# Kernel tuning notes

Hardware: AMD Instinct MI355X
Metric: run time of the kernel (lower is better)

The kernel has to match this reference:

```python
import jax, jax.numpy as jnp
import numpy as np

B, S, H = 512, 200, 256

def setup_inputs() -> dict:
    key = jax.random.key(0)
    ks = jax.random.split(key, 7)
    scale = 1.0 / np.sqrt(H)
    return {
        "all_memory": jax.random.normal(ks[0], (B, S, H), dtype=jnp.float32),
        "last_memory": jax.random.normal(ks[1], (B, H), dtype=jnp.float32),
        "U": jax.random.normal(ks[2], (H, H), dtype=jnp.float32) * scale,   # U_meta weight
        "W": jax.random.normal(ks[3], (H, H), dtype=jnp.float32) * scale,   # W_meta weight
        "V": jax.random.normal(ks[4], (H, 1), dtype=jnp.float32) * scale,   # V_meta weight (stored as [H,1])
        "MetaW": jax.random.normal(ks[5], (4, H), dtype=jnp.float32) * scale,  # Meta weight
        "Metab": jax.random.normal(ks[6], (4,), dtype=jnp.float32) * scale,    # Meta bias ('multiple' mode)
    }

def reference(all_memory, last_memory, U, W, V, MetaW, Metab):
    # U_meta(all_memory): [B,S,H]; W_meta(last_memory): [B,H] broadcast over S
    a = jnp.einsum('bsh,kh->bsk', all_memory, U)
    l = jnp.einsum('bh,kh->bk', last_memory, W)
    # additive attention score: V_meta(tanh(a + l)) -> [B,S]
    scores = jnp.einsum('bsh,h->bs', jnp.tanh(a + l[:, None, :]), V[:, 0])
    alpha = jax.nn.softmax(scores, axis=1)  # softmax over seq dim
    pooled = jnp.einsum('bs,bsh->bh', alpha, all_memory)  # weighted sum of values
    return pooled @ MetaW.T + Metab  # [B, 4]
```

## Files before the change

### kernel.cpp

```cpp
#include <hip/hip_runtime.h>
#include <hip/hip_bf16.h>
#include <math.h>

#define NB 512
#define NS 200
#define NH 256
#define TILE_S 32
#define LDSPAD 8
#define LDW (NH + LDSPAD)

#define OFF_L    0
#define OFF_UB   (NB * NH)
#define WS_FLOATS_PRE  (OFF_UB + (NH * NH) / 2)

typedef _Float16 f16x8 __attribute__((ext_vector_type(8)));
typedef float    f32x4 __attribute__((ext_vector_type(4)));

template<int CTRL>
__device__ __forceinline__ float dpp_xadd(float v) {
  return v + __int_as_float(
      __builtin_amdgcn_update_dpp(0, __float_as_int(v), CTRL, 0xf, 0xf, true));
}
__device__ __forceinline__ float row16_sum(float v) {
  v = dpp_xadd<0xB1>(v);
  v = dpp_xadd<0x4E>(v);
  v = dpp_xadd<0x124>(v);
  v = dpp_xadd<0x128>(v);
  return v;
}

__global__ __launch_bounds__(256)
void precompute(const float* __restrict__ lastm, const float* __restrict__ W,
                const float* __restrict__ U,
                float* __restrict__ l_ws, _Float16* __restrict__ Uswz)
{
  const int t = threadIdx.x;
  if (blockIdx.x < NB) {
    const int b = blockIdx.x;
    __shared__ float lm_sm[NH];
    lm_sm[t] = lastm[(size_t)b * NH + t];
    __syncthreads();
    const float4* wrow = (const float4*)(W + (size_t)t * NH);
    const float4* lrow = (const float4*)lm_sm;
    float a0 = 0.f, a1 = 0.f, a2 = 0.f, a3 = 0.f;
#pragma unroll 8
    for (int i = 0; i < NH / 4; ++i) {
      float4 w4 = wrow[i];
      float4 m4 = lrow[i];
      a0 = fmaf(w4.x, m4.x, a0);
      a1 = fmaf(w4.y, m4.y, a1);
      a2 = fmaf(w4.z, m4.z, a2);
      a3 = fmaf(w4.w, m4.w, a3);
    }
    l_ws[(size_t)b * NH + t] = (a0 + a1) + (a2 + a3);
  } else {
    const int id    = (blockIdx.x - NB) * 256 + t;
    const int n_blk = id >> 9;
    const int kk    = (id >> 6) & 7;
    const int lane  = id & 63;
    const int row   = n_blk * 16 + (lane & 15);
    const int col   = kk * 32 + (lane >> 4) * 8;
    const float4* s = (const float4*)(U + (size_t)row * NH + col);
    const float4 a = s[0], c = s[1];
    f16x8 pk;
    pk[0] = (_Float16)a.x; pk[1] = (_Float16)a.y;
    pk[2] = (_Float16)a.z; pk[3] = (_Float16)a.w;
    pk[4] = (_Float16)c.x; pk[5] = (_Float16)c.y;
    pk[6] = (_Float16)c.z; pk[7] = (_Float16)c.w;
    *(f16x8*)(Uswz + (size_t)id * 8) = pk;
  }
}

#define CVT_HL(idx, val) { const float x_ = (val); const _Float16 h_ = (_Float16)x_; \
                           ph[idx] = h_; pl[idx] = (_Float16)(x_ - (float)h_); }

template<bool PRE>
__global__ __launch_bounds__(512, 2)
void fused_attn(const float* __restrict__ mem,
                const float* __restrict__ lastm,
                const float* __restrict__ U,
                const float* __restrict__ W,
                const float* __restrict__ V,
                const float* __restrict__ l_ws,
                const _Float16* __restrict__ Uswz,
                const float* __restrict__ MetaW,
                const float* __restrict__ Metab,
                float* __restrict__ out)
{
  const int b = blockIdx.x;
  const int ntiles = 7;

  const int t     = threadIdx.x;
  const int wave  = t >> 6;
  const int lane  = t & 63;
  const int m16   = lane & 15;
  const int quad  = lane >> 4;
  const int g     = t >> 5;
  const int hblk  = (t & 31) * 8;

  __shared__ __align__(16) _Float16 hi_sm[2][TILE_S][LDW];
  __shared__ __align__(16) _Float16 lo_sm[2][TILE_S][LDW];
  __shared__ float swave_sm[8][TILE_S];
  __shared__ float e_sm[TILE_S];
  __shared__ float mz_sm[2];

  float l_reg[2], v_reg[2];
  if constexpr (!PRE) {
    __shared__ float l_sm[NH];
    __shared__ float lm_sm[NH];
    if (t < NH) lm_sm[t] = lastm[(size_t)b * NH + t];
    __syncthreads();
    if (t < NH) {
      const float4* wrow = (const float4*)(W + (size_t)t * NH);
      const float4* lrow = (const float4*)lm_sm;
      float a0 = 0.f, a1 = 0.f, a2 = 0.f, a3 = 0.f;
#pragma unroll 8
      for (int i = 0; i < NH / 4; ++i) {
        float4 w4 = wrow[i];
        float4 m4 = lrow[i];
        a0 = fmaf(w4.x, m4.x, a0);
        a1 = fmaf(w4.y, m4.y, a1);
        a2 = fmaf(w4.z, m4.z, a2);
        a3 = fmaf(w4.w, m4.w, a3);
      }
      l_sm[t] = (a0 + a1) + (a2 + a3);
    }
    __syncthreads();
#pragma unroll
    for (int nf = 0; nf < 2; ++nf)
      l_reg[nf] = l_sm[wave * 32 + nf * 16 + m16];
  } else {
#pragma unroll
    for (int nf = 0; nf < 2; ++nf)
      l_reg[nf] = l_ws[(size_t)b * NH + wave * 32 + nf * 16 + m16];
  }
#pragma unroll
  for (int nf = 0; nf < 2; ++nf)
    v_reg[nf] = V[wave * 32 + nf * 16 + m16];
  const float vsum  = v_reg[0] + v_reg[1];
  const float vm2_0 = -2.f * v_reg[0];
  const float vm2_1 = -2.f * v_reg[1];

  f16x8 u_frag[2][8];
  if constexpr (PRE) {
    const _Float16* uw = Uswz + ((size_t)(wave * 2 * 8 * 64) + lane) * 8;
#pragma unroll
    for (int nf = 0; nf < 2; ++nf)
#pragma unroll
      for (int kk = 0; kk < 8; ++kk)
        u_frag[nf][kk] = *(const f16x8*)(uw + (size_t)((nf * 8 + kk) << 9));
  } else {
#pragma unroll
    for (int nf = 0; nf < 2; ++nf) {
      const int n = wave * 32 + nf * 16 + m16;
      const float* urow = U + (size_t)n * NH;
#pragma unroll
      for (int kk = 0; kk < 8; ++kk) {
        const float4 lo = *(const float4*)(urow + kk * 32 + quad * 8);
        const float4 hi = *(const float4*)(urow + kk * 32 + quad * 8 + 4);
        f16x8 f;
        f[0] = (_Float16)lo.x; f[1] = (_Float16)lo.y;
        f[2] = (_Float16)lo.z; f[3] = (_Float16)lo.w;
        f[4] = (_Float16)hi.x; f[5] = (_Float16)hi.y;
        f[6] = (_Float16)hi.z; f[7] = (_Float16)hi.w;
        u_frag[nf][kk] = f;
      }
    }
  }

  {
    const float4* src4 = (const float4*)(mem + (size_t)b * NS * NH);
    const int f0 = t, f1 = 512 + t;
    const float4 a0 = src4[f0 * 2], a1 = src4[f0 * 2 + 1];
    const float4 b0 = src4[f1 * 2], b1 = src4[f1 * 2 + 1];
    {
      f16x8 ph, pl;
      CVT_HL(0, a0.x) CVT_HL(1, a0.y) CVT_HL(2, a0.z) CVT_HL(3, a0.w)
      CVT_HL(4, a1.x) CVT_HL(5, a1.y) CVT_HL(6, a1.z) CVT_HL(7, a1.w)
      *(f16x8*)&hi_sm[0][f0 >> 5][(f0 & 31) * 8] = ph;
      *(f16x8*)&lo_sm[0][f0 >> 5][(f0 & 31) * 8] = pl;
    }
    {
      f16x8 ph, pl;
      CVT_HL(0, b0.x) CVT_HL(1, b0.y) CVT_HL(2, b0.z) CVT_HL(3, b0.w)
      CVT_HL(4, b1.x) CVT_HL(5, b1.y) CVT_HL(6, b1.z) CVT_HL(7, b1.w)
      *(f16x8*)&hi_sm[0][f1 >> 5][(f1 & 31) * 8] = ph;
      *(f16x8*)&lo_sm[0][f1 >> 5][(f1 & 31) * 8] = pl;
    }
  }
  __syncthreads();

  float m_run = -INFINITY;
  float Z     = 0.f;
  float pooledv[8];
#pragma unroll
  for (int j = 0; j < 8; ++j) pooledv[j] = 0.f;

  for (int tile = 0; tile < ntiles; ++tile) {
    const int cur = tile & 1;
    const int nxt = cur ^ 1;
    const int s0  = tile * TILE_S;
    const int rows = min(TILE_S, NS - s0);
    const int rows_next = (tile + 1 < ntiles) ? min(TILE_S, NS - (s0 + TILE_S)) : 0;

    float4 p00, p01, p10, p11;
    const bool ld0 = (t >> 5) < rows_next;
    const bool ld1 = 16 + (t >> 5) < rows_next;
    {
      const float4* nsrc = (const float4*)(mem + ((size_t)b * NS + s0 + TILE_S) * NH);
      if (ld0) { p00 = nsrc[t * 2];         p01 = nsrc[t * 2 + 1]; }
      if (ld1) { p10 = nsrc[(512 + t) * 2]; p11 = nsrc[(512 + t) * 2 + 1]; }
    }

    f32x4 acc[2][2];
    const f32x4 fzero = {0.f, 0.f, 0.f, 0.f};
#pragma unroll
    for (int mt = 0; mt < 2; ++mt)
#pragma unroll
      for (int nf = 0; nf < 2; ++nf)
        acc[mt][nf] = fzero;

#pragma unroll
    for (int kk = 0; kk < 8; ++kk) {
      const int c = kk * 32 + quad * 8;
      f16x8 a0h = *(const f16x8*)&hi_sm[cur][m16][c];
      f16x8 a1h = *(const f16x8*)&hi_sm[cur][16 + m16][c];
      f16x8 a0l = *(const f16x8*)&lo_sm[cur][m16][c];
      f16x8 a1l = *(const f16x8*)&lo_sm[cur][16 + m16][c];
#pragma unroll
      for (int nf = 0; nf < 2; ++nf) {
        acc[0][nf] = __builtin_amdgcn_mfma_f32_16x16x32_f16(a0h, u_frag[nf][kk], acc[0][nf], 0, 0, 0);
        acc[1][nf] = __builtin_amdgcn_mfma_f32_16x16x32_f16(a1h, u_frag[nf][kk], acc[1][nf], 0, 0, 0);
        acc[0][nf] = __builtin_amdgcn_mfma_f32_16x16x32_f16(a0l, u_frag[nf][kk], acc[0][nf], 0, 0, 0);
        acc[1][nf] = __builtin_amdgcn_mfma_f32_16x16x32_f16(a1l, u_frag[nf][kk], acc[1][nf], 0, 0, 0);
      }
    }

#pragma unroll
    for (int mt = 0; mt < 2; ++mt) {
#pragma unroll
      for (int reg = 0; reg < 4; ++reg) {
        const float x0 = acc[mt][0][reg] + l_reg[0];
        const float x1 = acc[mt][1][reg] + l_reg[1];
        const float e0 = __expf(x0 + x0);
        const float e1 = __expf(x1 + x1);
        float s = vsum;
        s += __fdividef(vm2_0, e0 + 1.f);
        s += __fdividef(vm2_1, e1 + 1.f);
        s = row16_sum(s);
        if (m16 == 0)
          swave_sm[wave][mt * 16 + quad * 4 + reg] = s;
      }
    }
    __syncthreads();

    if (t < TILE_S) {
      float s = swave_sm[0][t];
#pragma unroll
      for (int w = 1; w < 8; ++w) s += swave_sm[w][t];
      const float sv = (t < rows) ? s : -INFINITY;
      float mt_ = sv;
#pragma unroll
      for (int off = 1; off < 32; off <<= 1)
        mt_ = fmaxf(mt_, __shfl_xor(mt_, off));
      const float m_new = fmaxf(m_run, mt_);
      float e = (t < rows) ? __expf(sv - m_new) : 0.f;
      e_sm[t] = e;
      float z = e;
#pragma unroll
      for (int off = 1; off < 32; off <<= 1)
        z += __shfl_xor(z, off);
      if (t == 0) { mz_sm[0] = m_new; mz_sm[1] = z; }
    }

    if (ld0) {
      f16x8 ph, pl;
      CVT_HL(0, p00.x) CVT_HL(1, p00.y) CVT_HL(2, p00.z) CVT_HL(3, p00.w)
      CVT_HL(4, p01.x) CVT_HL(5, p01.y) CVT_HL(6, p01.z) CVT_HL(7, p01.w)
      *(f16x8*)&hi_sm[nxt][t >> 5][(t & 31) * 8] = ph;
      *(f16x8*)&lo_sm[nxt][t >> 5][(t & 31) * 8] = pl;
    }
    if (ld1) {
      f16x8 ph, pl;
      CVT_HL(0, p10.x) CVT_HL(1, p10.y) CVT_HL(2, p10.z) CVT_HL(3, p10.w)
      CVT_HL(4, p11.x) CVT_HL(5, p11.y) CVT_HL(6, p11.z) CVT_HL(7, p11.w)
      *(f16x8*)&hi_sm[nxt][16 + (t >> 5)][(t & 31) * 8] = ph;
      *(f16x8*)&lo_sm[nxt][16 + (t >> 5)][(t & 31) * 8] = pl;
    }
    __syncthreads();

    const float m_new = mz_sm[0];
    const float z_new = mz_sm[1];
    const float fac   = __expf(m_run - m_new);
    m_run = m_new;
    Z = fmaf(Z, fac, z_new);

    const float e0 = e_sm[2 * g];
    const float e1 = e_sm[2 * g + 1];
    const f16x8 r0 = *(const f16x8*)&hi_sm[cur][2 * g][hblk];
    const f16x8 r1 = *(const f16x8*)&hi_sm[cur][2 * g + 1][hblk];
#pragma unroll
    for (int j = 0; j < 8; ++j)
      pooledv[j] = fmaf(e0, (float)r0[j], fmaf(e1, (float)r1[j], pooledv[j] * fac));
    __syncthreads();
  }

  float* scratch = (float*)&hi_sm[0][0][0];
  float* pooled_sm = (float*)&lo_sm[0][0][0];
  {
    f32x4 lo4 = {pooledv[0], pooledv[1], pooledv[2], pooledv[3]};
    f32x4 hi4 = {pooledv[4], pooledv[5], pooledv[6], pooledv[7]};
    *(f32x4*)&scratch[g * 264 + hblk]     = lo4;
    *(f32x4*)&scratch[g * 264 + hblk + 4] = hi4;
  }
  __syncthreads();
  const float Zi = 1.f / Z;
  if (t < NH) {
    float p = 0.f;
#pragma unroll
    for (int r = 0; r < 16; ++r)
      p += scratch[r * 264 + t];
    pooled_sm[t] = p * Zi;
  }
  __syncthreads();
  if (t < 256) {
    float s = 0.f;
#pragma unroll
    for (int i = 0; i < 4; ++i) {
      const int h = i * 64 + lane;
      s = fmaf(pooled_sm[h], MetaW[(size_t)wave * NH + h], s);
    }
#pragma unroll
    for (int off = 32; off > 0; off >>= 1)
      s += __shfl_down(s, off);
    if (lane == 0)
      out[b * 4 + wave] = s + Metab[wave];
  }
}

extern "C" void kernel_launch(void* const* d_in, const int* in_sizes, int n_in,
                              void* d_out, int out_size, void* d_ws, size_t ws_size,
                              hipStream_t stream) {
  const float* mem   = (const float*)d_in[0];
  const float* lastm = (const float*)d_in[1];
  const float* U     = (const float*)d_in[2];
  const float* W     = (const float*)d_in[3];
  const float* V     = (const float*)d_in[4];
  const float* MetaW = (const float*)d_in[5];
  const float* Metab = (const float*)d_in[6];
  float* out = (float*)d_out;
  float* ws  = (float*)d_ws;

  if (ws_size >= (size_t)WS_FLOATS_PRE * sizeof(float)) {
    float*    l_ws = ws + OFF_L;
    _Float16* Uswz = (_Float16*)(ws + OFF_UB);
    hipLaunchKernelGGL(precompute, dim3(NB + 32), dim3(256), 0, stream,
                       lastm, W, U, l_ws, Uswz);
    hipLaunchKernelGGL(fused_attn<true>, dim3(NB), dim3(512), 0, stream,
                       mem, lastm, U, W, V, l_ws, Uswz, MetaW, Metab, out);
  } else {
    hipLaunchKernelGGL(fused_attn<false>, dim3(NB), dim3(512), 0, stream,
                       mem, lastm, U, W, V, (const float*)nullptr, (const _Float16*)nullptr,
                       MetaW, Metab, out);
  }
}
```

Baseline: 200.7 us.

## Drop fp16 hi/lo split for memory tile and triple-buffer to remove a barrier

Stops splitting each memory element into fp16 high and low parts, so the MFMA score GEMM uses a single fp16 operand and issues half as many MFMAs and LDS reads and writes. Shared memory changes from two double-buffered hi/lo arrays to one triple-buffered array, which lets the trailing per-tile __syncthreads be removed. The cost is lower precision in the attention scores, since the fp16 rounding residual is no longer compensated. Correctness now relies on the triple buffer making that dropped barrier safe.

Result: no change. 204.3 us (+1.8%).

```diff
diff --git a/kernel.cpp b/kernel.cpp
--- a/kernel.cpp
+++ b/kernel.cpp
@@ -71,8 +71,10 @@
   }
 }
 
-#define CVT_HL(idx, val) { const float x_ = (val); const _Float16 h_ = (_Float16)x_; \
-                           ph[idx] = h_; pl[idx] = (_Float16)(x_ - (float)h_); }
+#define CVT8(ph, a, c) { ph[0] = (_Float16)a.x; ph[1] = (_Float16)a.y; \
+                         ph[2] = (_Float16)a.z; ph[3] = (_Float16)a.w; \
+                         ph[4] = (_Float16)c.x; ph[5] = (_Float16)c.y; \
+                         ph[6] = (_Float16)c.z; ph[7] = (_Float16)c.w; }
 
 template<bool PRE>
 __global__ __launch_bounds__(512, 2)
@@ -98,8 +100,7 @@
   const int g     = t >> 5;
   const int hblk  = (t & 31) * 8;
 
-  __shared__ __align__(16) _Float16 hi_sm[2][TILE_S][LDW];
-  __shared__ __align__(16) _Float16 lo_sm[2][TILE_S][LDW];
+  __shared__ __align__(16) _Float16 buf_sm[3][TILE_S][LDW];
   __shared__ float swave_sm[8][TILE_S];
   __shared__ float e_sm[TILE_S];
   __shared__ float mz_sm[2];
@@ -174,18 +175,14 @@
     const float4 a0 = src4[f0 * 2], a1 = src4[f0 * 2 + 1];
     const float4 b0 = src4[f1 * 2], b1 = src4[f1 * 2 + 1];
     {
-      f16x8 ph, pl;
-      CVT_HL(0, a0.x) CVT_HL(1, a0.y) CVT_HL(2, a0.z) CVT_HL(3, a0.w)
-      CVT_HL(4, a1.x) CVT_HL(5, a1.y) CVT_HL(6, a1.z) CVT_HL(7, a1.w)
-      *(f16x8*)&hi_sm[0][f0 >> 5][(f0 & 31) * 8] = ph;
-      *(f16x8*)&lo_sm[0][f0 >> 5][(f0 & 31) * 8] = pl;
+      f16x8 ph;
+      CVT8(ph, a0, a1)
+      *(f16x8*)&buf_sm[0][f0 >> 5][(f0 & 31) * 8] = ph;
     }
     {
-      f16x8 ph, pl;
-      CVT_HL(0, b0.x) CVT_HL(1, b0.y) CVT_HL(2, b0.z) CVT_HL(3, b0.w)
-      CVT_HL(4, b1.x) CVT_HL(5, b1.y) CVT_HL(6, b1.z) CVT_HL(7, b1.w)
-      *(f16x8*)&hi_sm[0][f1 >> 5][(f1 & 31) * 8] = ph;
-      *(f16x8*)&lo_sm[0][f1 >> 5][(f1 & 31) * 8] = pl;
+      f16x8 ph;
+      CVT8(ph, b0, b1)
+      *(f16x8*)&buf_sm[0][f1 >> 5][(f1 & 31) * 8] = ph;
     }
   }
   __syncthreads();
@@ -196,9 +193,9 @@
 #pragma unroll
   for (int j = 0; j < 8; ++j) pooledv[j] = 0.f;
 
+  int cur = 0;
   for (int tile = 0; tile < ntiles; ++tile) {
-    const int cur = tile & 1;
-    const int nxt = cur ^ 1;
+    const int nxt = (cur == 2) ? 0 : cur + 1;
     const int s0  = tile * TILE_S;
     const int rows = min(TILE_S, NS - s0);
     const int rows_next = (tile + 1 < ntiles) ? min(TILE_S, NS - (s0 + TILE_S)) : 0;
@@ -212,6 +209,7 @@
       if (ld1) { p10 = nsrc[(512 + t) * 2]; p11 = nsrc[(512 + t) * 2 + 1]; }
     }
 
+    const _Float16 (*bufc)[LDW] = buf_sm[cur];
     f32x4 acc[2][2];
     const f32x4 fzero = {0.f, 0.f, 0.f, 0.f};
 #pragma unroll
@@ -223,16 +221,12 @@
 #pragma unroll
     for (int kk = 0; kk < 8; ++kk) {
       const int c = kk * 32 + quad * 8;
-      f16x8 a0h = *(const f16x8*)&hi_sm[cur][m16][c];
-      f16x8 a1h = *(const f16x8*)&hi_sm[cur][16 + m16][c];
-      f16x8 a0l = *(const f16x8*)&lo_sm[cur][m16][c];
-      f16x8 a1l = *(const f16x8*)&lo_sm[cur][16 + m16][c];
+      f16x8 a0 = *(const f16x8*)&bufc[m16][c];
+      f16x8 a1 = *(const f16x8*)&bufc[16 + m16][c];
 #pragma unroll
       for (int nf = 0; nf < 2; ++nf) {
-        acc[0][nf] = __builtin_amdgcn_mfma_f32_16x16x32_f16(a0h, u_frag[nf][kk], acc[0][nf], 0, 0, 0);
-        acc[1][nf] = __builtin_amdgcn_mfma_f32_16x16x32_f16(a1h, u_frag[nf][kk], acc[1][nf], 0, 0, 0);
-        acc[0][nf] = __builtin_amdgcn_mfma_f32_16x16x32_f16(a0l, u_frag[nf][kk], acc[0][nf], 0, 0, 0);
-        acc[1][nf] = __builtin_amdgcn_mfma_f32_16x16x32_f16(a1l, u_frag[nf][kk], acc[1][nf], 0, 0, 0);
+        acc[0][nf] = __builtin_amdgcn_mfma_f32_16x16x32_f16(a0, u_frag[nf][kk], acc[0][nf], 0, 0, 0);
+        acc[1][nf] = __builtin_amdgcn_mfma_f32_16x16x32_f16(a1, u_frag[nf][kk], acc[1][nf], 0, 0, 0);
       }
     }
 
@@ -274,18 +268,14 @@
     }
 
     if (ld0) {
-      f16x8 ph, pl;
-      CVT_HL(0, p00.x) CVT_HL(1, p00.y) CVT_HL(2, p00.z) CVT_HL(3, p00.w)
-      CVT_HL(4, p01.x) CVT_HL(5, p01.y) CVT_HL(6, p01.z) CVT_HL(7, p01.w)
-      *(f16x8*)&hi_sm[nxt][t >> 5][(t & 31) * 8] = ph;
-      *(f16x8*)&lo_sm[nxt][t >> 5][(t & 31) * 8] = pl;
+      f16x8 ph;
+      CVT8(ph, p00, p01)
+      *(f16x8*)&buf_sm[nxt][t >> 5][(t & 31) * 8] = ph;
     }
     if (ld1) {
-      f16x8 ph, pl;
-      CVT_HL(0, p10.x) CVT_HL(1, p10.y) CVT_HL(2, p10.z) CVT_HL(3, p10.w)
-      CVT_HL(4, p11.x) CVT_HL(5, p11.y) CVT_HL(6, p11.z) CVT_HL(7, p11.w)
-      *(f16x8*)&hi_sm[nxt][16 + (t >> 5)][(t & 31) * 8] = ph;
-      *(f16x8*)&lo_sm[nxt][16 + (t >> 5)][(t & 31) * 8] = pl;
+      f16x8 ph;
+      CVT8(ph, p10, p11)
+      *(f16x8*)&buf_sm[nxt][16 + (t >> 5)][(t & 31) * 8] = ph;
     }
     __syncthreads();
 
@@ -297,16 +287,18 @@
 
     const float e0 = e_sm[2 * g];
     const float e1 = e_sm[2 * g + 1];
-    const f16x8 r0 = *(const f16x8*)&hi_sm[cur][2 * g][hblk];
-    const f16x8 r1 = *(const f16x8*)&hi_sm[cur][2 * g + 1][hblk];
+    const f16x8 r0 = *(const f16x8*)&buf_sm[cur][2 * g][hblk];
+    const f16x8 r1 = *(const f16x8*)&buf_sm[cur][2 * g + 1][hblk];
 #pragma unroll
     for (int j = 0; j < 8; ++j)
       pooledv[j] = fmaf(e0, (float)r0[j], fmaf(e1, (float)r1[j], pooledv[j] * fac));
-    __syncthreads();
-  }
-
-  float* scratch = (float*)&hi_sm[0][0][0];
-  float* pooled_sm = (float*)&lo_sm[0][0][0];
+
+    cur = nxt;
+  }
+  __syncthreads();
+
+  float* scratch   = (float*)&buf_sm[0][0][0];
+  float* pooled_sm = (float*)&buf_sm[1][0][0];
   {
     f32x4 lo4 = {pooledv[0], pooledv[1], pooledv[2], pooledv[3]};
     f32x4 hi4 = {pooledv[4], pooledv[5], pooledv[6], pooledv[7]};
```

## Prefetch global tiles two steps ahead and drop trailing per-tile barrier

Applied to the files above, without the earlier changes.

The register prefetch of the next sequence tile now runs two tiles ahead. The first prefetch is issued in the prologue, and each refill is issued right after the previous prefetched data is converted into LDS, so global loads overlap the pooling step and the next tile's MFMA work. The barrier at the end of each tile iteration is removed, leaving one barrier after the loop, which relies on later in-loop barriers to protect reuse of the LDS buffers. This cuts per-tile sync cost and load latency exposure, at the cost of keeping prefetch registers live across the whole iteration.

Result: no change. 197.5 us (-1.6%).

```diff
diff --git a/kernel.cpp b/kernel.cpp
--- a/kernel.cpp
+++ b/kernel.cpp
@@ -168,6 +168,7 @@
     }
   }
 
+  float4 q00, q01, q10, q11;
   {
     const float4* src4 = (const float4*)(mem + (size_t)b * NS * NH);
     const int f0 = t, f1 = 512 + t;
@@ -187,6 +188,9 @@
       *(f16x8*)&hi_sm[0][f1 >> 5][(f1 & 31) * 8] = ph;
       *(f16x8*)&lo_sm[0][f1 >> 5][(f1 & 31) * 8] = pl;
     }
+    const float4* nsrc = (const float4*)(mem + ((size_t)b * NS + TILE_S) * NH);
+    q00 = nsrc[t * 2];         q01 = nsrc[t * 2 + 1];
+    q10 = nsrc[(512 + t) * 2]; q11 = nsrc[(512 + t) * 2 + 1];
   }
   __syncthreads();
 
@@ -200,17 +204,9 @@
     const int cur = tile & 1;
     const int nxt = cur ^ 1;
     const int s0  = tile * TILE_S;
-    const int rows = min(TILE_S, NS - s0);
-    const int rows_next = (tile + 1 < ntiles) ? min(TILE_S, NS - (s0 + TILE_S)) : 0;
-
-    float4 p00, p01, p10, p11;
-    const bool ld0 = (t >> 5) < rows_next;
-    const bool ld1 = 16 + (t >> 5) < rows_next;
-    {
-      const float4* nsrc = (const float4*)(mem + ((size_t)b * NS + s0 + TILE_S) * NH);
-      if (ld0) { p00 = nsrc[t * 2];         p01 = nsrc[t * 2 + 1]; }
-      if (ld1) { p10 = nsrc[(512 + t) * 2]; p11 = nsrc[(512 + t) * 2 + 1]; }
-    }
+    const int rows   = min(TILE_S, NS - s0);
+    const int rows_w = (tile + 1 < ntiles) ? min(TILE_S, NS - (s0 + TILE_S)) : 0;
+    const int rows_i = (tile + 2 < ntiles) ? min(TILE_S, NS - (s0 + 2 * TILE_S)) : 0;
 
     f32x4 acc[2][2];
     const f32x4 fzero = {0.f, 0.f, 0.f, 0.f};
@@ -273,19 +269,25 @@
       if (t == 0) { mz_sm[0] = m_new; mz_sm[1] = z; }
     }
 
-    if (ld0) {
+    if ((t >> 5) < rows_w) {
       f16x8 ph, pl;
-      CVT_HL(0, p00.x) CVT_HL(1, p00.y) CVT_HL(2, p00.z) CVT_HL(3, p00.w)
-      CVT_HL(4, p01.x) CVT_HL(5, p01.y) CVT_HL(6, p01.z) CVT_HL(7, p01.w)
+      CVT_HL(0, q00.x) CVT_HL(1, q00.y) CVT_HL(2, q00.z) CVT_HL(3, q00.w)
+      CVT_HL(4, q01.x) CVT_HL(5, q01.y) CVT_HL(6, q01.z) CVT_HL(7, q01.w)
       *(f16x8*)&hi_sm[nxt][t >> 5][(t & 31) * 8] = ph;
       *(f16x8*)&lo_sm[nxt][t >> 5][(t & 31) * 8] = pl;
     }
-    if (ld1) {
+    if (16 + (t >> 5) < rows_w) {
       f16x8 ph, pl;
-      CVT_HL(0, p10.x) CVT_HL(1, p10.y) CVT_HL(2, p10.z) CVT_HL(3, p10.w)
-      CVT_HL(4, p11.x) CVT_HL(5, p11.y) CVT_HL(6, p11.z) CVT_HL(7, p11.w)
+      CVT_HL(0, q10.x) CVT_HL(1, q10.y) CVT_HL(2, q10.z) CVT_HL(3, q10.w)
+      CVT_HL(4, q11.x) CVT_HL(5, q11.y) CVT_HL(6, q11.z) CVT_HL(7, q11.w)
       *(f16x8*)&hi_sm[nxt][16 + (t >> 5)][(t & 31) * 8] = ph;
       *(f16x8*)&lo_sm[nxt][16 + (t >> 5)][(t & 31) * 8] = pl;
+    }
+
+    if (rows_i > 0) {
+      const float4* nsrc = (const float4*)(mem + ((size_t)b * NS + s0 + 2 * TILE_S) * NH);
+      if ((t >> 5) < rows_i)      { q00 = nsrc[t * 2];         q01 = nsrc[t * 2 + 1]; }
+      if (16 + (t >> 5) < rows_i) { q10 = nsrc[(512 + t) * 2]; q11 = nsrc[(512 + t) * 2 + 1]; }
     }
     __syncthreads();
 
@@ -302,10 +304,10 @@
 #pragma unroll
     for (int j = 0; j < 8; ++j)
       pooledv[j] = fmaf(e0, (float)r0[j], fmaf(e1, (float)r1[j], pooledv[j] * fac));
-    __syncthreads();
-  }
-
-  float* scratch = (float*)&hi_sm[0][0][0];
+  }
+  __syncthreads();
+
+  float* scratch   = (float*)&hi_sm[0][0][0];
   float* pooled_sm = (float*)&lo_sm[0][0][0];
   {
     f32x4 lo4 = {pooledv[0], pooledv[1], pooledv[2], pooledv[3]};
```
